# Kernel tuning notes

Measured on AMD Instinct MI355X. Metric: run time of the kernel, lower is better.

The kernel has to match this reference:

```python
import jax, jax.numpy as jnp
import numpy as np
import math

B, T, D = 4, 4096, 256


def setup_inputs() -> dict:
    key = jax.random.key(0)
    ks = jax.random.split(key, 12)
    stdv = 1.0 / math.sqrt(D)
    u = lambda k, shape, s: jax.random.uniform(k, shape, jnp.float32, -s, s)
    return {
        "query": jax.random.normal(ks[0], (B, T, D), jnp.float32),
        "value": jax.random.normal(ks[1], (B, T, D), jnp.float32),
        # gate vectors, init uniform(-1/sqrt(D), 1/sqrt(D)) per reset_parameters
        "q_vec": u(ks[2], (D,), stdv),
        "k_vec": u(ks[3], (D,), stdv),
        "v_vec": u(ks[4], (D,), stdv),
        # nn.Linear params (torch default init: uniform(-1/sqrt(fan_in), ...))
        "Wq": u(ks[5], (D, D), stdv), "bq": u(ks[6], (D,), stdv),
        "Ws": u(ks[7], (D, D), stdv), "bs": u(ks[8], (D,), stdv),
        "Wt": u(ks[9], (D, D), stdv), "bt": u(ks[10], (D,), stdv),
    }


def reference(query, value, q_vec, k_vec, v_vec, Wq, bq, Ws, bs, Wt, bt):
    d = query.shape[-1]
    # q = Linear(query) * sigmoid(query_vector)
    q = (jnp.einsum('btd,ed->bte', query, Wq) + bq) * jax.nn.sigmoid(q_vec)
    # k = value * sigmoid(key_vector)
    k = value * jax.nn.sigmoid(k_vec)
    # v gate: infer=False branch -> GLU-style gate of sigmoid(value_vector)
    vv = jax.nn.sigmoid(v_vec)
    v_gate = jax.nn.sigmoid(Ws @ vv + bs) * jnp.tanh(Wt @ vv + bt)
    v = value * v_gate
    # scores [B, T, T]
    w = jnp.einsum('bqd,bkd->bqk', q, k) / jnp.sqrt(jnp.float32(d))
    # causal: multiply by tril mask then replace exact zeros with -inf
    # (faithful to the original's weight[weight==0]=-inf quirk)
    Tn = w.shape[-1]
    tril = jnp.tril(jnp.ones((Tn, Tn), w.dtype))
    w = w * tril
    w = jnp.where(w == 0.0, -jnp.inf, w)
    attn = jax.nn.softmax(w, axis=-1)
    return jnp.einsum('bqk,bkd->bqd', attn, v)
```

## Files before the change

### kernel.cpp

```cpp
#include <hip/hip_runtime.h>
#include <math.h>

#define D 256
#define T 4096
#define KT (17408/2)
#define VT (20480/2)
#define PSTR ((size_t)4*T*D)

typedef __attribute__((ext_vector_type(8))) short bf16x8;
typedef __attribute__((ext_vector_type(4))) float f32x4;
typedef __attribute__((ext_vector_type(4))) unsigned short u16x4;

__device__ __forceinline__ unsigned short f2bf(float x){
  unsigned int u = __float_as_uint(x);
  unsigned int r = (u + 0x7FFFu + ((u >> 16) & 1u)) >> 16;
  return (unsigned short)r;
}
__device__ __forceinline__ float bf2f(unsigned short h){
  return __uint_as_float(((unsigned int)h) << 16);
}

__device__ __forceinline__ void gl_lds16(const void* g, void* l){
  __builtin_amdgcn_global_load_lds((const __attribute__((address_space(1))) unsigned int*)g,
                                   (__attribute__((address_space(3))) unsigned int*)l, 16, 0, 0);
}

__global__ __launch_bounds__(256) void prep_kernel(
    const float* __restrict__ q_vec, const float* __restrict__ k_vec,
    const float* __restrict__ v_vec, const float* __restrict__ Ws,
    const float* __restrict__ bs, const float* __restrict__ Wt,
    const float* __restrict__ bt, const float* __restrict__ Wq,
    float* __restrict__ gates, unsigned short* __restrict__ wq_g){
  int t = threadIdx.x;
  if(blockIdx.x == 0){
    __shared__ float vv[D];
    vv[t]         = 1.f/(1.f + __expf(-v_vec[t]));
    gates[t]      = 1.f/(1.f + __expf(-q_vec[t]));
    gates[D + t]  = 1.f/(1.f + __expf(-k_vec[t]));
    __syncthreads();
    const f32x4* wsr = (const f32x4*)(Ws + (size_t)t*D);
    const f32x4* wtr = (const f32x4*)(Wt + (size_t)t*D);
    const f32x4* vvv = (const f32x4*)vv;
    f32x4 a0 = {0,0,0,0}, a1 = {0,0,0,0}, c0 = {0,0,0,0}, c1 = {0,0,0,0};
    for(int i=0;i<64;i+=2){
      f32x4 v0 = vvv[i], v1 = vvv[i+1];
      a0 += wsr[i]*v0; a1 += wsr[i+1]*v1;
      c0 += wtr[i]*v0; c1 += wtr[i+1]*v1;
    }
    f32x4 as = a0 + a1, cs = c0 + c1;
    float s1 = bs[t] + as[0]+as[1]+as[2]+as[3];
    float s2 = bt[t] + cs[0]+cs[1]+cs[2]+cs[3];
    gates[2*D + t] = (1.f/(1.f + __expf(-s1))) * tanhf(s2);
  } else {
    int kc = blockIdx.x - 1;
    const float* src = Wq + (size_t)t*D + kc*32;
    unsigned short* dst = wq_g + (size_t)kc*10240 + t*40;
    #pragma unroll
    for(int u=0;u<4;u++){
      bf16x8 pk;
      #pragma unroll
      for(int x=0;x<8;x++) pk[x] = (short)f2bf(src[u*8+x]);
      *(bf16x8*)&dst[u*8] = pk;
    }
  }
}

__global__ __launch_bounds__(256) void mid_kernel(
    const float* __restrict__ query, const unsigned short* __restrict__ wq_g,
    const float* __restrict__ bq, const float* __restrict__ gates,
    unsigned short* __restrict__ q_g,
    const float* __restrict__ value,
    unsigned short* __restrict__ k_g, unsigned short* __restrict__ vt_g){
  __shared__ __align__(16) unsigned short smem[2][10240];
  int tid = threadIdx.x;
  if(blockIdx.x < 256){
    int w = tid >> 6; int l = tid & 63;
    int lr = l & 15, lc = l >> 4;
    int r0 = blockIdx.x * 64;
    f32x4 acc[16];
    #pragma unroll
    for(int n=0;n<16;n++) acc[n] = (f32x4){0.f,0.f,0.f,0.f};
    const float* qrow = query + (size_t)(r0 + w*16 + lr)*D;
    #pragma unroll
    for(int i=0;i<5;i++){ int c = i*256 + tid; gl_lds16(wq_g + c*8, (char*)smem[0] + c*16); }
    __syncthreads();
    int cur = 0;
    for(int kc=0; kc<8; kc++){
      if(kc < 7){
        #pragma unroll
        for(int i=0;i<5;i++){ int c = i*256 + tid;
          gl_lds16(wq_g + (size_t)(kc+1)*10240 + c*8, (char*)smem[cur^1] + c*16); }
      }
      bf16x8 af;
      {
        const float* s = qrow + kc*32 + lc*8;
        #pragma unroll
        for(int x=0;x<8;x++) af[x] = (short)f2bf(s[x]);
      }
      #pragma unroll
      for(int n=0;n<16;n++){
        bf16x8 bfrag = *(const bf16x8*)&smem[cur][(n*16 + lr)*40 + lc*8];
        acc[n] = __builtin_amdgcn_mfma_f32_16x16x32_bf16(af, bfrag, acc[n], 0, 0, 0);
      }
      __syncthreads();
      cur ^= 1;
    }
    #pragma unroll
    for(int n=0;n<16;n++){
      int col = n*16 + lr;
      float bb = bq[col], gg = gates[col];
      #pragma unroll
      for(int r=0;r<4;r++){
        int row = r0 + w*16 + lc*4 + r;
        q_g[(size_t)row*D + col] = f2bf((acc[n][r] + bb) * gg);
      }
    }
  } else {
    int bid2 = blockIdx.x - 256;
    int b = bid2 >> 7, jt = bid2 & 127;
    const float* vbase = value + ((size_t)b*T + jt*32)*D;
    const float* gk = gates + D;
    const float* vg = gates + 2*D;
    unsigned short* kt = k_g  + (size_t)bid2 * KT;
    unsigned short* vt = vt_g + (size_t)bid2 * VT;
    #pragma unroll
    for(int i=0;i<4;i++){
      int g = i*256 + tid; int j = g >> 5, c = g & 31;
      const float* src = vbase + j*D + c*8;
      bf16x8 pk;
      #pragma unroll
      for(int x=0;x<8;x++) pk[x] = (short)f2bf(src[x] * gk[c*8+x]);
      *(bf16x8*)&kt[j*264 + c*8] = pk;
    }
    float* lds = (float*)smem;
    for(int c=0;c<4;c++){
      __syncthreads();
      {
        int row = tid >> 3, cg = tid & 7;
        const float* src = vbase + (size_t)row*D + c*64 + cg*8;
        f32x4 v0 = *(const f32x4*)src;
        f32x4 v1 = *(const f32x4*)(src + 4);
        *(f32x4*)&lds[row*68 + cg*8]     = v0;
        *(f32x4*)&lds[row*68 + cg*8 + 4] = v1;
      }
      __syncthreads();
      {
        int d0l = tid >> 2, u = tid & 3;
        int d0 = c*64 + d0l;
        float gd = vg[d0];
        bf16x8 pk;
        #pragma unroll
        for(int x=0;x<8;x++){
          int p = u*8 + x;
          int ksrc = ((p>>3)<<2) + (p&3) + (((p>>2)&1)<<4);
          pk[x] = (short)f2bf(lds[ksrc*68 + d0l] * gd);
        }
        *(bf16x8*)&vt[d0*40 + u*8] = pk;
      }
    }
  }
}

__global__ __launch_bounds__(256, 2) void flash_kernel(
    const unsigned short* __restrict__ q_g,
    const unsigned short* __restrict__ k_g,
    const unsigned short* __restrict__ vt_g,
    unsigned short* __restrict__ parts,
    float* __restrict__ ml, int logS){
  __shared__ __align__(16) unsigned short kbuf[2][KT];
  __shared__ __align__(16) unsigned short vbuf[2][VT];
  int tid = threadIdx.x; int w = tid >> 6, l = tid & 63;
  int lr = l & 15, lc = l >> 4;
  int S = 1 << logS;
  int bid = blockIdx.x;
  int x = bid & 7; int b = x >> 1; int p = x & 1;
  int item = bid >> 3;
  int half = S >> 1;
  int rblk = 31 - (item / half);
  int s = p*half + (item % half);
  int r0 = rblk * 128;
  int wrow0 = r0 + w*32;
  int nt = 4*rblk + 4;
  int jt0 = (s*nt) >> logS, jt1 = ((s+1)*nt) >> logS;
  int grA = wrow0 + lr;
  int grB = wrow0 + 16 + lr;
  int diagA = (wrow0 + 15) >> 5;
  int diagB = (wrow0 + 31) >> 5;

  bf16x8 qfA[8], qfB[8];
  {
    const unsigned short* qa = q_g + ((size_t)b*T + grA)*D + lc*8;
    const unsigned short* qb = q_g + ((size_t)b*T + grB)*D + lc*8;
    #pragma unroll
    for(int kc=0;kc<8;kc++){
      qfA[kc] = *(const bf16x8*)(qa + kc*32);
      qfB[kc] = *(const bf16x8*)(qb + kc*32);
    }
  }
  f32x4 oA[16], oB[16];
  #pragma unroll
  for(int n=0;n<16;n++){ oA[n] = (f32x4){0.f,0.f,0.f,0.f}; oB[n] = (f32x4){0.f,0.f,0.f,0.f}; }
  float mA = -INFINITY, lsA = 0.f, mB = -INFINITY, lsB = 0.f;

  const unsigned short* ktb = k_g  + (size_t)b*128*KT;
  const unsigned short* vtb = vt_g + (size_t)b*128*VT;

  if(jt1 > jt0){
    const unsigned short* ks = ktb + (size_t)jt0*KT;
    const unsigned short* vs = vtb + (size_t)jt0*VT;
    for(int c=w; c<37; c+=4){
      if(c < 17) gl_lds16(ks + c*512 + l*8, (char*)kbuf[jt0&1] + c*1024);
      else       gl_lds16(vs + (c-17)*512 + l*8, (char*)vbuf[jt0&1] + (c-17)*1024);
    }
  }

  for(int jt=jt0; jt<jt1; jt++){
    int cur = jt & 1;
    asm volatile("s_waitcnt vmcnt(0)" ::: "memory");
    __builtin_amdgcn_s_barrier();
    __builtin_amdgcn_sched_barrier(0);
    if(jt+1 < jt1){
      const unsigned short* ks = ktb + (size_t)(jt+1)*KT;
      const unsigned short* vs = vtb + (size_t)(jt+1)*VT;
      for(int c=w; c<37; c+=4){
        if(c < 17) gl_lds16(ks + c*512 + l*8, (char*)kbuf[cur^1] + c*1024);
        else       gl_lds16(vs + (c-17)*512 + l*8, (char*)vbuf[cur^1] + (c-17)*1024);
      }
    }
    int j0 = jt*32;
    bool actA = (j0 <= wrow0 + 15);
    bool actB = (j0 <= wrow0 + 31);
    if(actB){
      f32x4 sA0={0,0,0,0}, sA1={0,0,0,0}, sB0={0,0,0,0}, sB1={0,0,0,0};
      if(actA){
        #pragma unroll
        for(int kc=0;kc<8;kc++){
          bf16x8 k0 = *(const bf16x8*)&kbuf[cur][lr*264        + (kc*4 + lc)*8];
          bf16x8 k1 = *(const bf16x8*)&kbuf[cur][(16 + lr)*264 + (kc*4 + lc)*8];
          sA0 = __builtin_amdgcn_mfma_f32_16x16x32_bf16(k0, qfA[kc], sA0, 0,0,0);
          sA1 = __builtin_amdgcn_mfma_f32_16x16x32_bf16(k1, qfA[kc], sA1, 0,0,0);
          sB0 = __builtin_amdgcn_mfma_f32_16x16x32_bf16(k0, qfB[kc], sB0, 0,0,0);
          sB1 = __builtin_amdgcn_mfma_f32_16x16x32_bf16(k1, qfB[kc], sB1, 0,0,0);
        }
      } else {
        #pragma unroll
        for(int kc=0;kc<8;kc++){
          bf16x8 k0 = *(const bf16x8*)&kbuf[cur][lr*264        + (kc*4 + lc)*8];
          bf16x8 k1 = *(const bf16x8*)&kbuf[cur][(16 + lr)*264 + (kc*4 + lc)*8];
          sB0 = __builtin_amdgcn_mfma_f32_16x16x32_bf16(k0, qfB[kc], sB0, 0,0,0);
          sB1 = __builtin_amdgcn_mfma_f32_16x16x32_bf16(k1, qfB[kc], sB1, 0,0,0);
        }
      }
      bf16x8 paA, paB;
      if(actA){
        float sv0[4], sv1[4];
        if(jt == diagA){
          #pragma unroll
          for(int r=0;r<4;r++){
            float x0 = sA0[r]*0.0625f; int gj0 = j0 + lc*4 + r;
            float x1 = sA1[r]*0.0625f; int gj1 = gj0 + 16;
            sv0[r] = (gj0 > grA || x0 == 0.0f) ? -INFINITY : x0;
            sv1[r] = (gj1 > grA || x1 == 0.0f) ? -INFINITY : x1;
          }
        } else {
          #pragma unroll
          for(int r=0;r<4;r++){
            float x0 = sA0[r]*0.0625f;
            float x1 = sA1[r]*0.0625f;
            sv0[r] = (x0 == 0.0f) ? -INFINITY : x0;
            sv1[r] = (x1 == 0.0f) ? -INFINITY : x1;
          }
        }
        float pmax = fmaxf(fmaxf(fmaxf(sv0[0],sv0[1]),fmaxf(sv0[2],sv0[3])),
                           fmaxf(fmaxf(sv1[0],sv1[1]),fmaxf(sv1[2],sv1[3])));
        pmax = fmaxf(pmax, __shfl_xor(pmax, 16));
        pmax = fmaxf(pmax, __shfl_xor(pmax, 32));
        bool mv = (pmax > mA + 8.0f);
        float mn = mv ? pmax : mA;
        float alpha = mv ? __expf(mA - mn) : 1.0f;
        float p0[4], p1[4];
        #pragma unroll
        for(int r=0;r<4;r++){
          p0[r] = __expf(sv0[r] - mn);
          p1[r] = __expf(sv1[r] - mn);
        }
        if(__builtin_amdgcn_ballot_w64(mv)){
          float a0 = __shfl(alpha, lc*4 + 0);
          float a1 = __shfl(alpha, lc*4 + 1);
          float a2 = __shfl(alpha, lc*4 + 2);
          float a3 = __shfl(alpha, lc*4 + 3);
          #pragma unroll
          for(int n=0;n<16;n++){
            oA[n][0] *= a0; oA[n][1] *= a1; oA[n][2] *= a2; oA[n][3] *= a3;
          }
        }
        float ps = ((p0[0]+p0[1])+(p0[2]+p0[3])) + ((p1[0]+p1[1])+(p1[2]+p1[3]));
        lsA = lsA*alpha + ps;
        mA = mn;
        #pragma unroll
        for(int r=0;r<4;r++){ paA[r] = (short)f2bf(p0[r]); paA[4+r] = (short)f2bf(p1[r]); }
      }
      {
        float sv0[4], sv1[4];
        if(jt == diagB){
          #pragma unroll
          for(int r=0;r<4;r++){
            float x0 = sB0[r]*0.0625f; int gj0 = j0 + lc*4 + r;
            float x1 = sB1[r]*0.0625f; int gj1 = gj0 + 16;
            sv0[r] = (gj0 > grB || x0 == 0.0f) ? -INFINITY : x0;
            sv1[r] = (gj1 > grB || x1 == 0.0f) ? -INFINITY : x1;
          }
        } else {
          #pragma unroll
          for(int r=0;r<4;r++){
            float x0 = sB0[r]*0.0625f;
            float x1 = sB1[r]*0.0625f;
            sv0[r] = (x0 == 0.0f) ? -INFINITY : x0;
            sv1[r] = (x1 == 0.0f) ? -INFINITY : x1;
          }
        }
        float pmax = fmaxf(fmaxf(fmaxf(sv0[0],sv0[1]),fmaxf(sv0[2],sv0[3])),
                           fmaxf(fmaxf(sv1[0],sv1[1]),fmaxf(sv1[2],sv1[3])));
        pmax = fmaxf(pmax, __shfl_xor(pmax, 16));
        pmax = fmaxf(pmax, __shfl_xor(pmax, 32));
        bool mv = (pmax > mB + 8.0f);
        float mn = mv ? pmax : mB;
        float alpha = mv ? __expf(mB - mn) : 1.0f;
        float p0[4], p1[4];
        #pragma unroll
        for(int r=0;r<4;r++){
          p0[r] = __expf(sv0[r] - mn);
          p1[r] = __expf(sv1[r] - mn);
        }
        if(__builtin_amdgcn_ballot_w64(mv)){
          float a0 = __shfl(alpha, lc*4 + 0);
          float a1 = __shfl(alpha, lc*4 + 1);
          float a2 = __shfl(alpha, lc*4 + 2);
          float a3 = __shfl(alpha, lc*4 + 3);
          #pragma unroll
          for(int n=0;n<16;n++){
            oB[n][0] *= a0; oB[n][1] *= a1; oB[n][2] *= a2; oB[n][3] *= a3;
          }
        }
        float ps = ((p0[0]+p0[1])+(p0[2]+p0[3])) + ((p1[0]+p1[1])+(p1[2]+p1[3]));
        lsB = lsB*alpha + ps;
        mB = mn;
        #pragma unroll
        for(int r=0;r<4;r++){ paB[r] = (short)f2bf(p0[r]); paB[4+r] = (short)f2bf(p1[r]); }
      }
      if(actA){
        #pragma unroll
        for(int n=0;n<16;n++){
          bf16x8 vf = *(const bf16x8*)&vbuf[cur][(n*16 + lr)*40 + lc*8];
          oA[n] = __builtin_amdgcn_mfma_f32_16x16x32_bf16(paA, vf, oA[n], 0,0,0);
          oB[n] = __builtin_amdgcn_mfma_f32_16x16x32_bf16(paB, vf, oB[n], 0,0,0);
        }
      } else {
        #pragma unroll
        for(int n=0;n<16;n++){
          bf16x8 vf = *(const bf16x8*)&vbuf[cur][(n*16 + lr)*40 + lc*8];
          oB[n] = __builtin_amdgcn_mfma_f32_16x16x32_bf16(paB, vf, oB[n], 0,0,0);
        }
      }
    }
  }

  unsigned short* obaseA = parts + (size_t)s*PSTR + ((size_t)b*T + wrow0)*D;
  unsigned short* obaseB = obaseA + (size_t)16*D;
  #pragma unroll
  for(int r=0;r<4;r++){
    #pragma unroll
    for(int n=0;n<16;n++){
      obaseA[(size_t)(lc*4 + r)*D + n*16 + lr] = f2bf(oA[n][r]);
      obaseB[(size_t)(lc*4 + r)*D + n*16 + lr] = f2bf(oB[n][r]);
    }
  }
  lsA += __shfl_xor(lsA, 16); lsA += __shfl_xor(lsA, 32);
  lsB += __shfl_xor(lsB, 16); lsB += __shfl_xor(lsB, 32);
  if(l < 16){
    float* mlbA = ml + ((size_t)s*4*T + (size_t)b*T + wrow0 + lr)*2;
    mlbA[0] = mA; mlbA[1] = lsA;
    float* mlbB = ml + ((size_t)s*4*T + (size_t)b*T + wrow0 + 16 + lr)*2;
    mlbB[0] = mB; mlbB[1] = lsB;
  }
}

__global__ __launch_bounds__(256) void combine_kernel(
    const unsigned short* __restrict__ parts, const float* __restrict__ ml,
    float* __restrict__ out, int S){
  size_t idx = (size_t)blockIdx.x*256 + threadIdx.x;
  size_t e = idx*4;
  size_t row = e >> 8;
  float msv[8], lsv[8];
  float mm = -INFINITY;
  for(int s=0;s<S;s++){
    msv[s] = ml[((size_t)s*4*T + row)*2];
    lsv[s] = ml[((size_t)s*4*T + row)*2 + 1];
    mm = fmaxf(mm, msv[s]);
  }
  float denom = 0.f;
  f32x4 acc = {0.f,0.f,0.f,0.f};
  for(int s=0;s<S;s++){
    float as = __expf(msv[s] - mm);
    if(as != 0.0f){
      denom += as*lsv[s];
      u16x4 v = *(const u16x4*)&parts[(size_t)s*PSTR + e];
      #pragma unroll
      for(int xx=0;xx<4;xx++) acc[xx] += as*bf2f(v[xx]);
    }
  }
  float inv = 1.0f/denom;
  f32x4 r;
  #pragma unroll
  for(int xx=0;xx<4;xx++) r[xx] = acc[xx]*inv;
  *(f32x4*)&out[e] = r;
}

extern "C" void kernel_launch(void* const* d_in, const int* in_sizes, int n_in,
                              void* d_out, int out_size, void* d_ws, size_t ws_size,
                              hipStream_t stream){
  (void)in_sizes; (void)n_in; (void)out_size;
  const float* query = (const float*)d_in[0];
  const float* value = (const float*)d_in[1];
  const float* q_vec = (const float*)d_in[2];
  const float* k_vec = (const float*)d_in[3];
  const float* v_vec = (const float*)d_in[4];
  const float* Wq    = (const float*)d_in[5];
  const float* bq    = (const float*)d_in[6];
  const float* Ws    = (const float*)d_in[7];
  const float* bs    = (const float*)d_in[8];
  const float* Wt    = (const float*)d_in[9];
  const float* bt    = (const float*)d_in[10];
  char* ws = (char*)d_ws;
  unsigned short* q_g  = (unsigned short*)(ws);
  unsigned short* k_g  = (unsigned short*)(ws + 8388608);
  unsigned short* vt_g = (unsigned short*)(ws + 17301504);
  unsigned short* wq_g = (unsigned short*)(ws + 27787264);
  float* gates         = (float*)(ws + 27951104);
  unsigned short* parts= (unsigned short*)(ws + 27955200);
  float* out = (float*)d_out;

  size_t base = 27955200;
  size_t mlsz = (size_t)8*4*T*2*4;
  int logS;
  if(ws_size >= base + 8*PSTR*2 + mlsz)      logS = 3;
  else if(ws_size >= base + 4*PSTR*2 + mlsz) logS = 2;
  else                                       logS = 1;
  int S = 1 << logS;
  float* ml = (float*)(ws + base + (size_t)S*PSTR*2);

  hipLaunchKernelGGL(prep_kernel, dim3(9),   dim3(256), 0, stream,
                     q_vec, k_vec, v_vec, Ws, bs, Wt, bt, Wq, gates, wq_g);
  hipLaunchKernelGGL(mid_kernel,  dim3(768), dim3(256), 0, stream,
                     query, wq_g, bq, gates, q_g, value, k_g, vt_g);
  hipLaunchKernelGGL(flash_kernel, dim3(128*S), dim3(256), 0, stream,
                     q_g, k_g, vt_g, parts, ml, logS);
  hipLaunchKernelGGL(combine_kernel, dim3((4*T*D/4)/256), dim3(256), 0, stream,
                     parts, ml, out, S);
}
```

Baseline: 119.9 us.

## Fold softmax scale into Q, use exp2, packed bf16 converts, vectorized partial stores

Folds 1/sqrt(D)*log2(e) into the Q projection gate so the flash loop drops the per-score multiply and uses exp2 instead of exp, and raises the lazy-rescale threshold to match base-2 units. Replaces scalar float-to-bf16 rounding with the hardware packed conversion instruction for P fragments and outputs. The partial-output store is permuted so each lane writes 16-byte contiguous chunks, and the combine kernel reads those chunks and scatters back to natural column order. The zero-score check now compares prescaled values, which keeps the original quirk equivalent up to rounding.

```diff
diff --git a/kernel.cpp b/kernel.cpp
--- a/kernel.cpp
+++ b/kernel.cpp
@@ -9,7 +9,10 @@
 
 typedef __attribute__((ext_vector_type(8))) short bf16x8;
 typedef __attribute__((ext_vector_type(4))) float f32x4;
-typedef __attribute__((ext_vector_type(4))) unsigned short u16x4;
+typedef __attribute__((ext_vector_type(8))) unsigned short u16x8;
+typedef __attribute__((ext_vector_type(4))) unsigned int u32x4;
+
+#define QSCALE 0.0901684850f
 
 __device__ __forceinline__ unsigned short f2bf(float x){
   unsigned int u = __float_as_uint(x);
@@ -18,6 +21,11 @@
 }
 __device__ __forceinline__ float bf2f(unsigned short h){
   return __uint_as_float(((unsigned int)h) << 16);
+}
+__device__ __forceinline__ unsigned int cvtpk(float lo, float hi){
+  unsigned int w;
+  asm("v_cvt_pk_bf16_f32 %0, %1, %2" : "=v"(w) : "v"(lo), "v"(hi));
+  return w;
 }
 
 __device__ __forceinline__ void gl_lds16(const void* g, void* l){
@@ -108,7 +116,7 @@
     #pragma unroll
     for(int n=0;n<16;n++){
       int col = n*16 + lr;
-      float bb = bq[col], gg = gates[col];
+      float bb = bq[col], gg = gates[col] * QSCALE;
       #pragma unroll
       for(int r=0;r<4;r++){
         int row = r0 + w*16 + lc*4 + r;
@@ -257,32 +265,30 @@
         if(jt == diagA){
           #pragma unroll
           for(int r=0;r<4;r++){
-            float x0 = sA0[r]*0.0625f; int gj0 = j0 + lc*4 + r;
-            float x1 = sA1[r]*0.0625f; int gj1 = gj0 + 16;
+            float x0 = sA0[r]; int gj0 = j0 + lc*4 + r;
+            float x1 = sA1[r]; int gj1 = gj0 + 16;
             sv0[r] = (gj0 > grA || x0 == 0.0f) ? -INFINITY : x0;
             sv1[r] = (gj1 > grA || x1 == 0.0f) ? -INFINITY : x1;
           }
         } else {
           #pragma unroll
           for(int r=0;r<4;r++){
-            float x0 = sA0[r]*0.0625f;
-            float x1 = sA1[r]*0.0625f;
-            sv0[r] = (x0 == 0.0f) ? -INFINITY : x0;
-            sv1[r] = (x1 == 0.0f) ? -INFINITY : x1;
+            sv0[r] = (sA0[r] == 0.0f) ? -INFINITY : sA0[r];
+            sv1[r] = (sA1[r] == 0.0f) ? -INFINITY : sA1[r];
           }
         }
         float pmax = fmaxf(fmaxf(fmaxf(sv0[0],sv0[1]),fmaxf(sv0[2],sv0[3])),
                            fmaxf(fmaxf(sv1[0],sv1[1]),fmaxf(sv1[2],sv1[3])));
         pmax = fmaxf(pmax, __shfl_xor(pmax, 16));
         pmax = fmaxf(pmax, __shfl_xor(pmax, 32));
-        bool mv = (pmax > mA + 8.0f);
+        bool mv = (pmax > mA + 11.5f);
         float mn = mv ? pmax : mA;
-        float alpha = mv ? __expf(mA - mn) : 1.0f;
+        float alpha = mv ? exp2f(mA - mn) : 1.0f;
         float p0[4], p1[4];
         #pragma unroll
         for(int r=0;r<4;r++){
-          p0[r] = __expf(sv0[r] - mn);
-          p1[r] = __expf(sv1[r] - mn);
+          p0[r] = exp2f(sv0[r] - mn);
+          p1[r] = exp2f(sv1[r] - mn);
         }
         if(__builtin_amdgcn_ballot_w64(mv)){
           float a0 = __shfl(alpha, lc*4 + 0);
@@ -297,40 +303,40 @@
         float ps = ((p0[0]+p0[1])+(p0[2]+p0[3])) + ((p1[0]+p1[1])+(p1[2]+p1[3]));
         lsA = lsA*alpha + ps;
         mA = mn;
-        #pragma unroll
-        for(int r=0;r<4;r++){ paA[r] = (short)f2bf(p0[r]); paA[4+r] = (short)f2bf(p1[r]); }
+        union { unsigned int u[4]; bf16x8 h; } pu;
+        pu.u[0] = cvtpk(p0[0], p0[1]); pu.u[1] = cvtpk(p0[2], p0[3]);
+        pu.u[2] = cvtpk(p1[0], p1[1]); pu.u[3] = cvtpk(p1[2], p1[3]);
+        paA = pu.h;
       }
       {
         float sv0[4], sv1[4];
         if(jt == diagB){
           #pragma unroll
           for(int r=0;r<4;r++){
-            float x0 = sB0[r]*0.0625f; int gj0 = j0 + lc*4 + r;
-            float x1 = sB1[r]*0.0625f; int gj1 = gj0 + 16;
+            float x0 = sB0[r]; int gj0 = j0 + lc*4 + r;
+            float x1 = sB1[r]; int gj1 = gj0 + 16;
             sv0[r] = (gj0 > grB || x0 == 0.0f) ? -INFINITY : x0;
             sv1[r] = (gj1 > grB || x1 == 0.0f) ? -INFINITY : x1;
           }
         } else {
           #pragma unroll
           for(int r=0;r<4;r++){
-            float x0 = sB0[r]*0.0625f;
-            float x1 = sB1[r]*0.0625f;
-            sv0[r] = (x0 == 0.0f) ? -INFINITY : x0;
-            sv1[r] = (x1 == 0.0f) ? -INFINITY : x1;
+            sv0[r] = (sB0[r] == 0.0f) ? -INFINITY : sB0[r];
+            sv1[r] = (sB1[r] == 0.0f) ? -INFINITY : sB1[r];
           }
         }
         float pmax = fmaxf(fmaxf(fmaxf(sv0[0],sv0[1]),fmaxf(sv0[2],sv0[3])),
                            fmaxf(fmaxf(sv1[0],sv1[1]),fmaxf(sv1[2],sv1[3])));
         pmax = fmaxf(pmax, __shfl_xor(pmax, 16));
         pmax = fmaxf(pmax, __shfl_xor(pmax, 32));
-        bool mv = (pmax > mB + 8.0f);
+        bool mv = (pmax > mB + 11.5f);
         float mn = mv ? pmax : mB;
-        float alpha = mv ? __expf(mB - mn) : 1.0f;
+        float alpha = mv ? exp2f(mB - mn) : 1.0f;
         float p0[4], p1[4];
         #pragma unroll
         for(int r=0;r<4;r++){
-          p0[r] = __expf(sv0[r] - mn);
-          p1[r] = __expf(sv1[r] - mn);
+          p0[r] = exp2f(sv0[r] - mn);
+          p1[r] = exp2f(sv1[r] - mn);
         }
         if(__builtin_amdgcn_ballot_w64(mv)){
           float a0 = __shfl(alpha, lc*4 + 0);
@@ -345,8 +351,10 @@
         float ps = ((p0[0]+p0[1])+(p0[2]+p0[3])) + ((p1[0]+p1[1])+(p1[2]+p1[3]));
         lsB = lsB*alpha + ps;
         mB = mn;
-        #pragma unroll
-        for(int r=0;r<4;r++){ paB[r] = (short)f2bf(p0[r]); paB[4+r] = (short)f2bf(p1[r]); }
+        union { unsigned int u[4]; bf16x8 h; } pu;
+        pu.u[0] = cvtpk(p0[0], p0[1]); pu.u[1] = cvtpk(p0[2], p0[3]);
+        pu.u[2] = cvtpk(p1[0], p1[1]); pu.u[3] = cvtpk(p1[2], p1[3]);
+        paB = pu.h;
       }
       if(actA){
         #pragma unroll
@@ -365,15 +373,20 @@
     }
   }
 
-  unsigned short* obaseA = parts + (size_t)s*PSTR + ((size_t)b*T + wrow0)*D;
-  unsigned short* obaseB = obaseA + (size_t)16*D;
+  unsigned short* obase = parts + (size_t)s*PSTR + ((size_t)b*T + wrow0)*D;
   #pragma unroll
   for(int r=0;r<4;r++){
-    #pragma unroll
-    for(int n=0;n<16;n++){
-      obaseA[(size_t)(lc*4 + r)*D + n*16 + lr] = f2bf(oA[n][r]);
-      obaseB[(size_t)(lc*4 + r)*D + n*16 + lr] = f2bf(oB[n][r]);
-    }
+    int row = lc*4 + r;
+    unsigned int wa[8], wb[8];
+    #pragma unroll
+    for(int k=0;k<8;k++){
+      wa[k] = cvtpk(oA[2*k][r], oA[2*k+1][r]);
+      wb[k] = cvtpk(oB[2*k][r], oB[2*k+1][r]);
+    }
+    *(u32x4*)&obase[(size_t)row*D + lr*16]          = (u32x4){wa[0],wa[1],wa[2],wa[3]};
+    *(u32x4*)&obase[(size_t)row*D + lr*16 + 8]      = (u32x4){wa[4],wa[5],wa[6],wa[7]};
+    *(u32x4*)&obase[(size_t)(row+16)*D + lr*16]     = (u32x4){wb[0],wb[1],wb[2],wb[3]};
+    *(u32x4*)&obase[(size_t)(row+16)*D + lr*16 + 8] = (u32x4){wb[4],wb[5],wb[6],wb[7]};
   }
   lsA += __shfl_xor(lsA, 16); lsA += __shfl_xor(lsA, 32);
   lsB += __shfl_xor(lsB, 16); lsB += __shfl_xor(lsB, 32);
@@ -388,32 +401,39 @@
 __global__ __launch_bounds__(256) void combine_kernel(
     const unsigned short* __restrict__ parts, const float* __restrict__ ml,
     float* __restrict__ out, int S){
-  size_t idx = (size_t)blockIdx.x*256 + threadIdx.x;
-  size_t e = idx*4;
-  size_t row = e >> 8;
+  int t = blockIdx.x*256 + threadIdx.x;
+  int row = t >> 4;
+  int lr  = t & 15;
   float msv[8], lsv[8];
   float mm = -INFINITY;
-  for(int s=0;s<S;s++){
+  #pragma unroll
+  for(int s=0;s<8;s++){
+    if(s >= S) break;
     msv[s] = ml[((size_t)s*4*T + row)*2];
     lsv[s] = ml[((size_t)s*4*T + row)*2 + 1];
     mm = fmaxf(mm, msv[s]);
   }
   float denom = 0.f;
-  f32x4 acc = {0.f,0.f,0.f,0.f};
-  for(int s=0;s<S;s++){
-    float as = __expf(msv[s] - mm);
+  float acc[16];
+  #pragma unroll
+  for(int n=0;n<16;n++) acc[n] = 0.f;
+  #pragma unroll
+  for(int s=0;s<8;s++){
+    if(s >= S) break;
+    float as = exp2f(msv[s] - mm);
     if(as != 0.0f){
       denom += as*lsv[s];
-      u16x4 v = *(const u16x4*)&parts[(size_t)s*PSTR + e];
+      const unsigned short* src = parts + (size_t)s*PSTR + (size_t)row*D + lr*16;
+      u16x8 v0 = *(const u16x8*)src;
+      u16x8 v1 = *(const u16x8*)(src + 8);
       #pragma unroll
-      for(int xx=0;xx<4;xx++) acc[xx] += as*bf2f(v[xx]);
+      for(int n=0;n<8;n++){ acc[n] += as*bf2f(v0[n]); acc[8+n] += as*bf2f(v1[n]); }
     }
   }
   float inv = 1.0f/denom;
-  f32x4 r;
-  #pragma unroll
-  for(int xx=0;xx<4;xx++) r[xx] = acc[xx]*inv;
-  *(f32x4*)&out[e] = r;
+  float* orow = out + (size_t)row*D;
+  #pragma unroll
+  for(int n=0;n<16;n++) orow[n*16 + lr] = acc[n]*inv;
 }
 
 extern "C" void kernel_launch(void* const* d_in, const int* in_sizes, int n_in,
@@ -455,6 +475,6 @@
                      query, wq_g, bq, gates, q_g, value, k_g, vt_g);
   hipLaunchKernelGGL(flash_kernel, dim3(128*S), dim3(256), 0, stream,
                      q_g, k_g, vt_g, parts, ml, logS);
-  hipLaunchKernelGGL(combine_kernel, dim3((4*T*D/4)/256), dim3(256), 0, stream,
+  hipLaunchKernelGGL(combine_kernel, dim3((4*T*16)/256), dim3(256), 0, stream,
                      parts, ml, out, S);
 }
```

Measured after the change: 113.6 us (median of 2 runs). 1.06x faster.
